# Performance work log

Hardware: AMD Instinct MI355X
Metric: run time of the kernel (lower is better)

Reference implementation:

```python
import jax, jax.numpy as jnp
import numpy as np

BETA = 0.25  # args.beta
B, T, D, K = 16, 4096, 64, 1024


def setup_inputs() -> dict:
    key = jax.random.key(0)
    kz, kw = jax.random.split(key)
    z = jax.random.normal(kz, (B, T, D), dtype=jnp.float32)
    # nn.Embedding weight init: uniform(-1/K, 1/K)
    emb = jax.random.uniform(kw, (K, D), dtype=jnp.float32,
                             minval=-1.0 / K, maxval=1.0 / K)
    return {"z": z, "emb": emb}


def reference(z, emb):
    # z: [B, T, D] (torch code loops over first dim; all elements non-empty here)
    # emb: [K, D] codebook
    b, t, d = z.shape
    zf = z.reshape(-1, d)                                   # [B*T, D]
    # squared euclidean distances: ||z||^2 + ||e||^2 - 2 z.e
    dist = (jnp.sum(zf * zf, axis=1, keepdims=True)
            + jnp.sum(emb * emb, axis=1)
            - 2.0 * zf @ emb.T)                             # [B*T, K]
    idx = jnp.argmin(dist, axis=1).reshape(b, t)            # [B, T] int
    z_q_raw = emb[idx]                                      # [B, T, D] gather
    sg = jax.lax.stop_gradient
    # per-batch-element means, summed (loop accumulates loss per z_t)
    commit = jnp.mean((sg(z_q_raw) - z) ** 2, axis=(1, 2))  # [B]
    codebk = jnp.mean((z_q_raw - sg(z)) ** 2, axis=(1, 2))  # [B]
    loss = jnp.sum(BETA * commit + codebk)
    # straight-through estimator
    z_q = z + sg(z_q_raw - z)
    return z_q, loss, idx
```

## Files before the change

### kernel.cpp

```cpp
#include <hip/hip_runtime.h>
#include <math.h>
#include <float.h>

#define NROWS    65536
#define DD       64
#define KK       1024
#define LOSS_OFF 4194304
#define IDX_OFF  4194305
#define RPB      64
#define MAXC     32
#define TPR      4
#define NRND     16

typedef short  short8 __attribute__((ext_vector_type(8)));
typedef float  f32x4  __attribute__((ext_vector_type(4)));

__device__ __forceinline__ void async_copy16(void* lds, const void* g) {
    __builtin_amdgcn_global_load_lds(
        (const __attribute__((address_space(1))) unsigned int*)g,
        (__attribute__((address_space(3))) unsigned int*)lds, 16, 0, 0);
}

__device__ __forceinline__ unsigned short bf16rne(float x) {
    unsigned int u = __float_as_uint(x);
    return (unsigned short)((u + 0x7fffu + ((u >> 16) & 1u)) >> 16);
}

__device__ __forceinline__ float np_acc8(const float* p, int j) {
#pragma clang fp contract(off)
    float r = 0.f;
#pragma unroll
    for (int i = 0; i < 8; ++i) {
        const float v = p[8 * i + j];
        r += v * v;
    }
    return r;
}

__global__ void vq_prep(const float* __restrict__ emb,
                        float* __restrict__ bn,
                        unsigned short* __restrict__ ebf) {
#pragma clang fp contract(off)
    const int gtid = blockIdx.x * 256 + threadIdx.x;
    const int code = gtid >> 3;
    const int j    = gtid & 7;
    const float* ep = emb + (size_t)code * DD;
    float r = 0.f;
#pragma unroll
    for (int i = 0; i < 8; ++i) {
        const float v = ep[8 * i + j];
        r += v * v;
    }
    const float s1 = r  + __shfl_xor(r,  1, 64);
    const float s2 = s1 + __shfl_xor(s1, 2, 64);
    const float s3 = s2 + __shfl_xor(s2, 4, 64);
    if (j == 0) bn[code] = s3;

    const float* cp = emb + (size_t)gtid * 8;
    const float4 u0 = *reinterpret_cast<const float4*>(cp);
    const float4 u1 = *reinterpret_cast<const float4*>(cp + 4);
    short8 s;
    s[0] = (short)bf16rne(u0.x); s[1] = (short)bf16rne(u0.y);
    s[2] = (short)bf16rne(u0.z); s[3] = (short)bf16rne(u0.w);
    s[4] = (short)bf16rne(u1.x); s[5] = (short)bf16rne(u1.y);
    s[6] = (short)bf16rne(u1.z); s[7] = (short)bf16rne(u1.w);
    const int g    = code >> 4;
    const int c16s = code & 15;
    const int half = j >> 2;
    const int qq   = j & 3;
    const size_t doff = (size_t)g * 1024 + half * 512 + (qq * 16 + c16s) * 8;
    *reinterpret_cast<short8*>(ebf + doff) = s;
}

__global__ __launch_bounds__(256)
void vq_main(const float* __restrict__ z, const float* __restrict__ emb,
             const unsigned short* __restrict__ ebf,
             const float* __restrict__ bn, float* __restrict__ out) {
    __shared__ char  dbuf[2][TPR * 2048] __attribute__((aligned(16)));
    __shared__ float a_s[RPB];
    __shared__ float bn_s[KK];
    __shared__ int   cnt[RPB];
    __shared__ int   clist[RPB][MAXC];
    __shared__ int   bidx[RPB];
    __shared__ double lsum[4];

    const int tid  = threadIdx.x;
    const int lane = tid & 63;
    const int wv   = __builtin_amdgcn_readfirstlane(tid) >> 6;
    const int q    = lane >> 4;
    const int c16  = lane & 15;
    const int rowbase = blockIdx.x * RPB;

    const char* sbase = (const char*)ebf + (size_t)lane * 16;
    char* dst0 = &dbuf[0][wv * 2048 + lane * 16];
    char* dst1 = &dbuf[1][wv * 2048 + lane * 16];

    {
        const int j8 = tid & 7;
#pragma unroll
        for (int sw = 0; sw < 2; ++sw) {
            const int rowl = 32 * sw + (tid >> 3);
            const float r = np_acc8(z + (size_t)(rowbase + rowl) * DD, j8);
            const float s1 = r  + __shfl_xor(r,  1, 64);
            const float s2 = s1 + __shfl_xor(s1, 2, 64);
            const float s3 = s2 + __shfl_xor(s2, 4, 64);
            if (j8 == 0) a_s[rowl] = s3;
        }
    }
    if (tid < RPB) cnt[tid] = 0;
    {
        const int i = tid * 4;
        *reinterpret_cast<float4*>(&bn_s[i]) =
            *reinterpret_cast<const float4*>(bn + i);
    }

    short8 afr[2];
#pragma unroll
    for (int kh = 0; kh < 2; ++kh) {
        const float* zp = z + (size_t)(rowbase + 16 * wv + c16) * DD
                          + 32 * kh + 8 * q;
        const float4 u0 = *reinterpret_cast<const float4*>(zp);
        const float4 u1 = *reinterpret_cast<const float4*>(zp + 4);
        short8 s;
        s[0] = (short)bf16rne(u0.x); s[1] = (short)bf16rne(u0.y);
        s[2] = (short)bf16rne(u0.z); s[3] = (short)bf16rne(u0.w);
        s[4] = (short)bf16rne(u1.x); s[5] = (short)bf16rne(u1.y);
        s[6] = (short)bf16rne(u1.z); s[7] = (short)bf16rne(u1.w);
        afr[kh] = s;
    }

    auto stage = [&](int R, int buf) {
        const char* s0 = sbase + (size_t)(TPR * R + wv) * 2048;
        char* d = buf ? dst1 : dst0;
        async_copy16(d,        s0);
        async_copy16(d + 1024, s0 + 1024);
    };

    stage(0, 0);
    __syncthreads();

    float wadd[4];
#pragma unroll
    for (int i = 0; i < 4; ++i) {
        const int rowl = 16 * wv + 4 * q + i;
        wadd[i] = 1.8e-4f * sqrtf(a_s[rowl]) + 1.2e-4f;
    }

    float mn[4];
#pragma unroll
    for (int i = 0; i < 4; ++i) mn[i] = FLT_MAX;

    for (int R = 0; R < NRND; ++R) {
        const int cur = R & 1;
        if (R < NRND - 1) stage(R + 1, cur ^ 1);
        float dv[TPR][4];
#pragma unroll
        for (int j = 0; j < TPR; ++j) {
            const char* tb = &dbuf[cur][j * 2048 + lane * 16];
            const short8 b0 = *reinterpret_cast<const short8*>(tb);
            const short8 b1 = *reinterpret_cast<const short8*>(tb + 1024);
            f32x4 acc = {0.f, 0.f, 0.f, 0.f};
            acc = __builtin_amdgcn_mfma_f32_16x16x32_bf16(afr[0], b0, acc, 0, 0, 0);
            acc = __builtin_amdgcn_mfma_f32_16x16x32_bf16(afr[1], b1, acc, 0, 0, 0);
            const float bnv = bn_s[16 * (TPR * R + j) + c16];
#pragma unroll
            for (int r = 0; r < 4; ++r)
                dv[j][r] = fmaf(-2.f, acc[r], bnv);
        }
#pragma unroll
        for (int j = 0; j < TPR; ++j)
#pragma unroll
            for (int r = 0; r < 4; ++r)
                mn[r] = fminf(mn[r], dv[j][r]);
#pragma unroll
        for (int mask = 1; mask < 16; mask <<= 1)
#pragma unroll
            for (int r = 0; r < 4; ++r)
                mn[r] = fminf(mn[r], __shfl_xor(mn[r], mask, 64));
        float thr[4];
#pragma unroll
        for (int r = 0; r < 4; ++r) thr[r] = mn[r] + wadd[r];
#pragma unroll
        for (int j = 0; j < TPR; ++j) {
            const int col = 16 * (TPR * R + j) + c16;
#pragma unroll
            for (int r = 0; r < 4; ++r) {
                if (dv[j][r] <= thr[r]) {
                    const int rowl = 16 * wv + 4 * q + r;
                    const int slot = atomicAdd(&cnt[rowl], 1);
                    if (slot < MAXC) clist[rowl][slot] = col;
                }
            }
        }
        __syncthreads();
    }

    {
        const int rowl = 16 * wv + c16;
        const int row  = rowbase + rowl;
        const int nc   = cnt[rowl];
        const bool full = nc > MAXC;
        const int lim  = full ? KK : nc;
        const float av = a_s[rowl];
        const float* zp = z + (size_t)row * DD;
        float sb = FLT_MAX;
        int   cb = 0x7fffffff;
        for (int jj = q; jj < lim; jj += 4) {
            const int c = full ? jj : clist[rowl][jj];
            const float* ep = emb + (size_t)c * DD;
            float dot = 0.f;
#pragma unroll
            for (int d = 0; d < DD; d += 4) {
                const float4 zv = *reinterpret_cast<const float4*>(zp + d);
                const float4 ev = *reinterpret_cast<const float4*>(ep + d);
                dot = fmaf(zv.x, ev.x, dot); dot = fmaf(zv.y, ev.y, dot);
                dot = fmaf(zv.z, ev.z, dot); dot = fmaf(zv.w, ev.w, dot);
            }
            const float tt = av + bn_s[c];
            const float sd = fmaf(-2.f, dot, tt);
            if (sd < sb || (sd == sb && c < cb)) { sb = sd; cb = c; }
        }
#pragma unroll
        for (int mask = 16; mask < 64; mask <<= 1) {
            const float so = __shfl_xor(sb, mask, 64);
            const int   co = __shfl_xor(cb, mask, 64);
            if (so < sb || (so == sb && co < cb)) { sb = so; cb = co; }
        }
        if (cb > 1023) cb = 0;
        if (q == 0) bidx[rowl] = cb;
    }
    __syncthreads();

    {
        const int rowl = tid >> 2;
        const int sub  = tid & 3;
        const int row  = rowbase + rowl;
        const int bid  = bidx[rowl];
        const float* ep = emb + (size_t)bid * DD + sub * 16;
        const float* zp = z + (size_t)row * DD + sub * 16;
        float* op = out + (size_t)row * DD + sub * 16;
        double sac = 0.0;
#pragma unroll
        for (int d = 0; d < 16; d += 4) {
            const float4 zv = *reinterpret_cast<const float4*>(zp + d);
            const float4 e4 = *reinterpret_cast<const float4*>(ep + d);
            const float df0 = e4.x - zv.x;
            const float df1 = e4.y - zv.y;
            const float df2 = e4.z - zv.z;
            const float df3 = e4.w - zv.w;
            float4 qv;
            qv.x = zv.x + df0; qv.y = zv.y + df1;
            qv.z = zv.z + df2; qv.w = zv.w + df3;
            *reinterpret_cast<float4*>(op + d) = qv;
            sac += (double)(df0 * df0); sac += (double)(df1 * df1);
            sac += (double)(df2 * df2); sac += (double)(df3 * df3);
        }
        if (sub == 0) out[IDX_OFF + row] = (float)bid;

        sac += __shfl_down(sac, 1, 64);
        sac += __shfl_down(sac, 2, 64);
        double v = (sub == 0) ? sac : 0.0;
#pragma unroll
        for (int off = 32; off > 0; off >>= 1) v += __shfl_down(v, off, 64);
        if (lane == 0) lsum[wv] = v;
    }
    __syncthreads();
    if (tid == 0)
        atomicAdd(&out[LOSS_OFF],
                  (float)((1.25 * (lsum[0] + lsum[1] + lsum[2] + lsum[3]))
                          / 262144.0));
}

extern "C" void kernel_launch(void* const* d_in, const int* in_sizes, int n_in,
                              void* d_out, int out_size, void* d_ws, size_t ws_size,
                              hipStream_t stream) {
    const float* z   = (const float*)d_in[0];
    const float* emb = (const float*)d_in[1];
    float* out = (float*)d_out;

    float*          bnw = (float*)d_ws;
    unsigned short* ebf = (unsigned short*)((char*)d_ws + 4096);

    vq_prep<<<dim3(32), dim3(256), 0, stream>>>(emb, bnw, ebf);
    vq_main<<<dim3(NROWS / RPB), dim3(256), 0, stream>>>(z, emb, ebf, bnw, out);
}
```

Baseline: 125.3 us.

## Stream codebook tiles directly into registers per wave, dropping LDS staging and barriers

The shared LDS double buffer, filled with async global-to-LDS copies and drained after a block-wide barrier every round, is removed. Each wave now loads every bf16 codebook tile and its norm straight from global memory into registers, double-buffered in two chunks so the next loads overlap the MFMAs on the current ones. The per-round __syncthreads is dropped and launch bounds ask for 4 blocks per CU. Each wave now reads the whole codebook itself, roughly four times the L2 traffic, and register pressure is higher in exchange for no cross-wave synchronisation.

```diff
diff --git a/kernel.cpp b/kernel.cpp
--- a/kernel.cpp
+++ b/kernel.cpp
@@ -9,17 +9,9 @@
 #define IDX_OFF  4194305
 #define RPB      64
 #define MAXC     32
-#define TPR      4
-#define NRND     16
 
 typedef short  short8 __attribute__((ext_vector_type(8)));
 typedef float  f32x4  __attribute__((ext_vector_type(4)));
-
-__device__ __forceinline__ void async_copy16(void* lds, const void* g) {
-    __builtin_amdgcn_global_load_lds(
-        (const __attribute__((address_space(1))) unsigned int*)g,
-        (__attribute__((address_space(3))) unsigned int*)lds, 16, 0, 0);
-}
 
 __device__ __forceinline__ unsigned short bf16rne(float x) {
     unsigned int u = __float_as_uint(x);
@@ -72,11 +64,10 @@
     *reinterpret_cast<short8*>(ebf + doff) = s;
 }
 
-__global__ __launch_bounds__(256)
+__global__ __launch_bounds__(256, 4)
 void vq_main(const float* __restrict__ z, const float* __restrict__ emb,
              const unsigned short* __restrict__ ebf,
              const float* __restrict__ bn, float* __restrict__ out) {
-    __shared__ char  dbuf[2][TPR * 2048] __attribute__((aligned(16)));
     __shared__ float a_s[RPB];
     __shared__ float bn_s[KK];
     __shared__ int   cnt[RPB];
@@ -91,9 +82,7 @@
     const int c16  = lane & 15;
     const int rowbase = blockIdx.x * RPB;
 
-    const char* sbase = (const char*)ebf + (size_t)lane * 16;
-    char* dst0 = &dbuf[0][wv * 2048 + lane * 16];
-    char* dst1 = &dbuf[1][wv * 2048 + lane * 16];
+    const char* ebase = (const char*)ebf + (size_t)lane * 16;
 
     {
         const int j8 = tid & 7;
@@ -129,14 +118,6 @@
         afr[kh] = s;
     }
 
-    auto stage = [&](int R, int buf) {
-        const char* s0 = sbase + (size_t)(TPR * R + wv) * 2048;
-        char* d = buf ? dst1 : dst0;
-        async_copy16(d,        s0);
-        async_copy16(d + 1024, s0 + 1024);
-    };
-
-    stage(0, 0);
     __syncthreads();
 
     float wadd[4];
@@ -146,32 +127,50 @@
         wadd[i] = 1.8e-4f * sqrtf(a_s[rowl]) + 1.2e-4f;
     }
 
+    auto loadChunk = [&](int c, short8 (&S)[4], float (&bnv)[2]) {
+        const char* t0 = ebase + (size_t)c * 4096;
+        S[0] = *reinterpret_cast<const short8*>(t0);
+        S[1] = *reinterpret_cast<const short8*>(t0 + 1024);
+        S[2] = *reinterpret_cast<const short8*>(t0 + 2048);
+        S[3] = *reinterpret_cast<const short8*>(t0 + 3072);
+        bnv[0] = bn[32 * c + c16];
+        bnv[1] = bn[32 * c + 16 + c16];
+    };
+    auto compute2 = [&](const short8 (&S)[4], const float (&bnv)[2],
+                        float (*dvt)[4]) {
+#pragma unroll
+        for (int t = 0; t < 2; ++t) {
+            f32x4 acc = {0.f, 0.f, 0.f, 0.f};
+            acc = __builtin_amdgcn_mfma_f32_16x16x32_bf16(afr[0], S[2*t],   acc, 0, 0, 0);
+            acc = __builtin_amdgcn_mfma_f32_16x16x32_bf16(afr[1], S[2*t+1], acc, 0, 0, 0);
+#pragma unroll
+            for (int r = 0; r < 4; ++r)
+                dvt[t][r] = fmaf(-2.f, acc[r], bnv[t]);
+        }
+    };
+
+    short8 SA[4], SB[4];
+    float  bnA[2], bnB[2];
+    loadChunk(0, SA, bnA);
+    loadChunk(1, SB, bnB);
+
     float mn[4];
 #pragma unroll
     for (int i = 0; i < 4; ++i) mn[i] = FLT_MAX;
 
-    for (int R = 0; R < NRND; ++R) {
-        const int cur = R & 1;
-        if (R < NRND - 1) stage(R + 1, cur ^ 1);
-        float dv[TPR][4];
-#pragma unroll
-        for (int j = 0; j < TPR; ++j) {
-            const char* tb = &dbuf[cur][j * 2048 + lane * 16];
-            const short8 b0 = *reinterpret_cast<const short8*>(tb);
-            const short8 b1 = *reinterpret_cast<const short8*>(tb + 1024);
-            f32x4 acc = {0.f, 0.f, 0.f, 0.f};
-            acc = __builtin_amdgcn_mfma_f32_16x16x32_bf16(afr[0], b0, acc, 0, 0, 0);
-            acc = __builtin_amdgcn_mfma_f32_16x16x32_bf16(afr[1], b1, acc, 0, 0, 0);
-            const float bnv = bn_s[16 * (TPR * R + j) + c16];
+#pragma unroll 4
+    for (int kp = 0; kp < 16; ++kp) {
+        float dvt[4][4];
+        compute2(SA, bnA, &dvt[0]);
+        if (kp < 15) loadChunk(2 * kp + 2, SA, bnA);
+        compute2(SB, bnB, &dvt[2]);
+        if (kp < 15) loadChunk(2 * kp + 3, SB, bnB);
+
+#pragma unroll
+        for (int j = 0; j < 4; ++j)
 #pragma unroll
             for (int r = 0; r < 4; ++r)
-                dv[j][r] = fmaf(-2.f, acc[r], bnv);
-        }
-#pragma unroll
-        for (int j = 0; j < TPR; ++j)
-#pragma unroll
-            for (int r = 0; r < 4; ++r)
-                mn[r] = fminf(mn[r], dv[j][r]);
+                mn[r] = fminf(mn[r], dvt[j][r]);
 #pragma unroll
         for (int mask = 1; mask < 16; mask <<= 1)
 #pragma unroll
@@ -181,18 +180,17 @@
 #pragma unroll
         for (int r = 0; r < 4; ++r) thr[r] = mn[r] + wadd[r];
 #pragma unroll
-        for (int j = 0; j < TPR; ++j) {
-            const int col = 16 * (TPR * R + j) + c16;
+        for (int j = 0; j < 4; ++j) {
+            const int col = 16 * (4 * kp + j) + c16;
 #pragma unroll
             for (int r = 0; r < 4; ++r) {
-                if (dv[j][r] <= thr[r]) {
+                if (dvt[j][r] <= thr[r]) {
                     const int rowl = 16 * wv + 4 * q + r;
                     const int slot = atomicAdd(&cnt[rowl], 1);
                     if (slot < MAXC) clist[rowl][slot] = col;
                 }
             }
         }
-        __syncthreads();
     }
 
     {
```

New measurement: 119.0 us. 5.0% less time.
